# Optimization experiments

Measured on AMD Instinct MI355X. Metric: run time of the kernel, lower is better.

The kernel has to match this reference:

```python
import jax, jax.numpy as jnp
import numpy as np

B, N, IN_DIM, HID = 8, 4096, 256, 256


def setup_inputs() -> dict:
    key = jax.random.key(0)
    ks = jax.random.split(key, 7)
    s_in = 1.0 / np.sqrt(IN_DIM)
    return {
        "x": jax.random.normal(ks[0], (B, N, IN_DIM), dtype=jnp.float32),
        "Wq": jax.random.uniform(ks[1], (IN_DIM, HID), jnp.float32, -s_in, s_in),
        "bq": jax.random.uniform(ks[2], (HID,), jnp.float32, -s_in, s_in),
        "Wk": jax.random.uniform(ks[3], (IN_DIM, HID), jnp.float32, -s_in, s_in),
        "bk": jax.random.uniform(ks[4], (HID,), jnp.float32, -s_in, s_in),
        "Wv": jax.random.uniform(ks[5], (IN_DIM, HID), jnp.float32, -s_in, s_in),
        "bv": jax.random.uniform(ks[6], (HID,), jnp.float32, -s_in, s_in),
    }


def reference(x, Wq, bq, Wk, bk, Wv, bv):
    # x: [B, N, in_dim]
    Q = jnp.einsum("bnd,dh->bnh", x, Wq) + bq  # [B, N, H]
    K = jnp.einsum("bnd,dh->bnh", x, Wk) + bk
    V = jnp.einsum("bnd,dh->bnh", x, Wv) + bv
    scale = 1.0 / jnp.sqrt(jnp.asarray(K.shape[-1], dtype=x.dtype))
    scores = jnp.einsum("bqh,bkh->bqk", Q, K) * scale  # [B, N, N]
    attn = jax.nn.softmax(scores, axis=-1)
    out = jnp.einsum("bqk,bkh->bqh", attn, V)  # [B, N, H]
    return out.mean(axis=1)  # [B, H]
```

## Files before the change

kernel.cpp:

```cpp
#include <hip/hip_runtime.h>
#include <hip/hip_bf16.h>


#define NTOK 4096
#define HDIM 256
#define NBATCH 8
#define SCALE 0.0625f

typedef __attribute__((ext_vector_type(8))) short short8_t;
typedef __attribute__((ext_vector_type(16))) float f32x16;

__device__ __forceinline__ unsigned short f2bf(float f) {
    unsigned u = __float_as_uint(f);
    u += 0x7fff + ((u >> 16) & 1);
    return (unsigned short)(u >> 16);
}

#define MFMA(a, b, c) __builtin_amdgcn_mfma_f32_32x32x16_bf16(a, b, c, 0, 0, 0)

__device__ __forceinline__ void async_cp16(const void* g, void* l) {
    __builtin_amdgcn_global_load_lds((const __attribute__((address_space(1))) void*)g,
                                     (__attribute__((address_space(3))) void*)l, 16, 0, 0);
}

__device__ __forceinline__ void stage_swz(unsigned short* lds, const unsigned short* src,
                                          int row0, int dbase, int w, int l) {
#pragma unroll
    for (int i = 0; i < 4; ++i) {
        int rloc = w * 32 + i * 8 + (l >> 3);
        int u = (l & 7) ^ (l >> 3);
        const unsigned short* g = src + (size_t)(row0 + rloc) * HDIM + dbase + u * 8;
        unsigned short* d = lds + (w * 32 + i * 8) * 64;
        async_cp16(g, d);
    }
}

__device__ __forceinline__ short8_t frd(const unsigned short* lds, int rb, int lo, int u) {
    return *(const short8_t*)(lds + ((rb * 32 + lo) * 8 + (u ^ (lo & 7))) * 8);
}

__global__ void zero_kernel(float* __restrict__ w, float* __restrict__ l, float* __restrict__ out) {
    int i = blockIdx.x * 256 + threadIdx.x;
    w[i] = 0.f;
    l[i] = 0.f;
    if (i < NBATCH * HDIM) out[i] = 0.f;
}

__global__ void convert_wt(const float* __restrict__ Wq, const float* __restrict__ Wk,
                           const float* __restrict__ Wv, unsigned short* __restrict__ Wt) {
    int z = blockIdx.y;
    const float* W = (z == 0) ? Wq : (z == 1) ? Wk : Wv;
    unsigned short* o = Wt + z * 65536;
    int n = threadIdx.x;
    for (int kk = 0; kk < 32; ++kk) {
        int k = blockIdx.x * 32 + kk;
        o[n * 256 + k] = f2bf(W[k * 256 + n]);
    }
}

__device__ __forceinline__ void stage_tile(unsigned short* __restrict__ dst,
                                           const unsigned short* __restrict__ src,
                                           int row0, int dbase, int t) {
#pragma unroll
    for (int i = 0; i < 4; ++i) {
        int f = t + i * 256;
        int r = f >> 3;
        int c8 = (f & 7) * 8;
        *(uint4*)(dst + r * 72 + c8) = *(const uint4*)(src + (size_t)(row0 + r) * HDIM + dbase + c8);
    }
}

__global__ __launch_bounds__(256) void qkv_mfma(const float* __restrict__ x,
                                                const unsigned short* __restrict__ Wt,
                                                const float* __restrict__ bq, const float* __restrict__ bk,
                                                const float* __restrict__ bv,
                                                unsigned short* __restrict__ Qbf,
                                                unsigned short* __restrict__ Kbf,
                                                float* __restrict__ Vf) {
    const int z = blockIdx.z;
    const unsigned short* Wz = Wt + z * 65536;
    const float* bias = (z == 0) ? bq : (z == 1) ? bk : bv;
    const int m0 = blockIdx.x * 128, n0 = blockIdx.y * 128;
    const int t = threadIdx.x, wv_ = t >> 6, l = t & 63, lo = l & 31, hi = l >> 5;
    const int wq = (wv_ & 1) * 64, wk = (wv_ >> 1) * 64;

    __shared__ __align__(16) char smem[36864];
    unsigned short* Xs = (unsigned short*)smem;
    unsigned short* Ws = Xs + 128 * 72;

    f32x16 acc[2][2];
#pragma unroll
    for (int a = 0; a < 2; ++a)
#pragma unroll
        for (int b = 0; b < 2; ++b)
#pragma unroll
            for (int r = 0; r < 16; ++r) acc[a][b][r] = 0.f;

    for (int dc = 0; dc < 4; ++dc) {
        __syncthreads();
#pragma unroll
        for (int i = 0; i < 4; ++i) {
            int f = t + i * 256;
            int r = f >> 3;
            int c8 = (f & 7) * 8;
            const float* s = x + (size_t)(m0 + r) * HDIM + dc * 64 + c8;
            float4 v0 = *(const float4*)s;
            float4 v1 = *(const float4*)(s + 4);
            short8_t o;
            o[0] = (short)f2bf(v0.x); o[1] = (short)f2bf(v0.y);
            o[2] = (short)f2bf(v0.z); o[3] = (short)f2bf(v0.w);
            o[4] = (short)f2bf(v1.x); o[5] = (short)f2bf(v1.y);
            o[6] = (short)f2bf(v1.z); o[7] = (short)f2bf(v1.w);
            *(short8_t*)(Xs + r * 72 + c8) = o;
        }
        stage_tile(Ws, Wz, n0, dc * 64, t);
        __syncthreads();
#pragma unroll
        for (int ks = 0; ks < 4; ++ks) {
            int kidx = ks * 16 + hi * 8;
            short8_t a0 = *(const short8_t*)(Xs + (wq + lo) * 72 + kidx);
            short8_t a1 = *(const short8_t*)(Xs + (wq + 32 + lo) * 72 + kidx);
            short8_t b0 = *(const short8_t*)(Ws + (wk + lo) * 72 + kidx);
            short8_t b1 = *(const short8_t*)(Ws + (wk + 32 + lo) * 72 + kidx);
            acc[0][0] = MFMA(a0, b0, acc[0][0]);
            acc[0][1] = MFMA(a0, b1, acc[0][1]);
            acc[1][0] = MFMA(a1, b0, acc[1][0]);
            acc[1][1] = MFMA(a1, b1, acc[1][1]);
        }
    }
    float bc0 = bias[n0 + wk + lo];
    float bc1 = bias[n0 + wk + 32 + lo];
#pragma unroll
    for (int mb = 0; mb < 2; ++mb)
#pragma unroll
        for (int r = 0; r < 16; ++r) {
            int row = m0 + wq + mb * 32 + (r & 3) + 8 * (r >> 2) + 4 * hi;
            int c0 = n0 + wk + lo, c1 = n0 + wk + 32 + lo;
            float v0 = acc[mb][0][r] + bc0;
            float v1 = acc[mb][1][r] + bc1;
            if (z == 2) {
                Vf[(size_t)row * HDIM + c0] = v0;
                Vf[(size_t)row * HDIM + c1] = v1;
            } else {
                unsigned short* o = (z == 0) ? Qbf : Kbf;
                o[(size_t)row * HDIM + c0] = f2bf(v0);
                o[(size_t)row * HDIM + c1] = f2bf(v1);
            }
        }
}

__global__ __launch_bounds__(256) void score_pass1(const unsigned short* __restrict__ Qbf,
                                                   const unsigned short* __restrict__ Kbf,
                                                   float* __restrict__ lsum) {
    const int b = blockIdx.z;
    const int q0 = blockIdx.x * 128;
    const int kslice = blockIdx.y;
    const int t = threadIdx.x, w = t >> 6, l = t & 63, lo = l & 31, hi = l >> 5;
    const int rq = (w & 1) * 2, rk = (w >> 1) * 2;
    const unsigned short* Qb = Qbf + (size_t)b * NTOK * HDIM;
    const unsigned short* Kb = Kbf + (size_t)b * NTOK * HDIM;

    __shared__ __align__(16) char smem[33792];
    unsigned short* Qs = (unsigned short*)smem;
    unsigned short* Ks = Qs + 8192;
    float* red = (float*)smem;

    float rs[2][16];
#pragma unroll
    for (int mb = 0; mb < 2; ++mb)
#pragma unroll
        for (int r = 0; r < 16; ++r) rs[mb][r] = 0.f;

    for (int kt = 0; kt < 4; ++kt) {
        const int k0 = kslice * 512 + kt * 128;
        f32x16 acc[2][2];
#pragma unroll
        for (int a = 0; a < 2; ++a)
#pragma unroll
            for (int c = 0; c < 2; ++c)
#pragma unroll
                for (int r = 0; r < 16; ++r) acc[a][c][r] = 0.f;

        for (int dc = 0; dc < 4; ++dc) {
            __syncthreads();
            stage_swz(Qs, Qb, q0, dc * 64, w, l);
            stage_swz(Ks, Kb, k0, dc * 64, w, l);
            __syncthreads();
#pragma unroll
            for (int ks = 0; ks < 4; ++ks) {
                int u = ks * 2 + hi;
                short8_t a0 = frd(Qs, rq + 0, lo, u);
                short8_t a1 = frd(Qs, rq + 1, lo, u);
                short8_t b0 = frd(Ks, rk + 0, lo, u);
                short8_t b1 = frd(Ks, rk + 1, lo, u);
                acc[0][0] = MFMA(a0, b0, acc[0][0]);
                acc[0][1] = MFMA(a0, b1, acc[0][1]);
                acc[1][0] = MFMA(a1, b0, acc[1][0]);
                acc[1][1] = MFMA(a1, b1, acc[1][1]);
            }
        }
#pragma unroll
        for (int mb = 0; mb < 2; ++mb)
#pragma unroll
            for (int r = 0; r < 16; ++r)
                rs[mb][r] += __expf(acc[mb][0][r] * SCALE) + __expf(acc[mb][1][r] * SCALE);
    }
    __syncthreads();
#pragma unroll
    for (int mb = 0; mb < 2; ++mb)
#pragma unroll
        for (int r = 0; r < 16; ++r) {
            int row = (w & 1) * 64 + mb * 32 + (r & 3) + 8 * (r >> 2) + 4 * hi;
            red[row * 66 + (w >> 1) * 32 + lo] = rs[mb][r];
        }
    __syncthreads();
    if (t < 128) {
        float s = 0.f;
#pragma unroll 8
        for (int j = 0; j < 64; ++j) s += red[t * 66 + j];
        atomicAdd(&lsum[b * NTOK + q0 + t], s);
    }
}

__global__ __launch_bounds__(256) void score_pass2(const unsigned short* __restrict__ Qbf,
                                                   const unsigned short* __restrict__ Kbf,
                                                   const float* __restrict__ lsum,
                                                   float* __restrict__ wsum) {
    const int b = blockIdx.z;
    const int k0 = blockIdx.x * 128;
    const int qslice = blockIdx.y;
    const int t = threadIdx.x, w = t >> 6, l = t & 63, lo = l & 31, hi = l >> 5;
    const int rq = (w & 1) * 2, rk = (w >> 1) * 2;
    const unsigned short* Qb = Qbf + (size_t)b * NTOK * HDIM;
    const unsigned short* Kb = Kbf + (size_t)b * NTOK * HDIM;

    __shared__ __align__(16) char smem[33792];
    __shared__ float linv_s[128];
    unsigned short* Qs = (unsigned short*)smem;
    unsigned short* Ks = Qs + 8192;
    float* red2 = (float*)smem;

    float cs0 = 0.f, cs1 = 0.f;

    for (int qt = 0; qt < 4; ++qt) {
        const int q0 = qslice * 512 + qt * 128;
        f32x16 acc[2][2];
#pragma unroll
        for (int a = 0; a < 2; ++a)
#pragma unroll
            for (int c = 0; c < 2; ++c)
#pragma unroll
                for (int r = 0; r < 16; ++r) acc[a][c][r] = 0.f;

        for (int dc = 0; dc < 4; ++dc) {
            __syncthreads();
            stage_swz(Qs, Qb, q0, dc * 64, w, l);
            stage_swz(Ks, Kb, k0, dc * 64, w, l);
            if (dc == 0 && t < 128) linv_s[t] = 1.0f / lsum[b * NTOK + q0 + t];
            __syncthreads();
#pragma unroll
            for (int ks = 0; ks < 4; ++ks) {
                int u = ks * 2 + hi;
                short8_t a0 = frd(Qs, rq + 0, lo, u);
                short8_t a1 = frd(Qs, rq + 1, lo, u);
                short8_t b0 = frd(Ks, rk + 0, lo, u);
                short8_t b1 = frd(Ks, rk + 1, lo, u);
                acc[0][0] = MFMA(a0, b0, acc[0][0]);
                acc[0][1] = MFMA(a0, b1, acc[0][1]);
                acc[1][0] = MFMA(a1, b0, acc[1][0]);
                acc[1][1] = MFMA(a1, b1, acc[1][1]);
            }
        }
#pragma unroll
        for (int mb = 0; mb < 2; ++mb)
#pragma unroll
            for (int r = 0; r < 16; ++r) {
                float li = linv_s[(w & 1) * 64 + mb * 32 + (r & 3) + 8 * (r >> 2) + 4 * hi];
                cs0 += __expf(acc[mb][0][r] * SCALE) * li;
                cs1 += __expf(acc[mb][1][r] * SCALE) * li;
            }
    }
    __syncthreads();
    red2[((w >> 1) * 64 + lo) * 5 + (w & 1) * 2 + hi] = cs0;
    red2[((w >> 1) * 64 + 32 + lo) * 5 + (w & 1) * 2 + hi] = cs1;
    __syncthreads();
    if (t < 128) {
        float s = red2[t * 5 + 0] + red2[t * 5 + 1] + red2[t * 5 + 2] + red2[t * 5 + 3];
        atomicAdd(&wsum[b * NTOK + k0 + t], s);
    }
}

__global__ __launch_bounds__(256) void finalize_kernel(const float* __restrict__ V,
                                                       const float* __restrict__ w,
                                                       float* __restrict__ out) {
    const int b = blockIdx.y;
    const int k0 = blockIdx.x * 256;
    const int h = threadIdx.x;
    __shared__ float wsh[256];
    wsh[h] = w[b * NTOK + k0 + h];
    __syncthreads();
    const float* Vb = V + ((size_t)b * NTOK + k0) * HDIM;
    float acc = 0.f;
#pragma unroll 4
    for (int kk = 0; kk < 256; ++kk) acc = fmaf(wsh[kk], Vb[(size_t)kk * HDIM + h], acc);
    atomicAdd(&out[b * HDIM + h], acc * (1.0f / (float)NTOK));
}

extern "C" void kernel_launch(void* const* d_in, const int* in_sizes, int n_in,
                              void* d_out, int out_size, void* d_ws, size_t ws_size,
                              hipStream_t stream) {
    const float* x  = (const float*)d_in[0];
    const float* Wq = (const float*)d_in[1];
    const float* bq = (const float*)d_in[2];
    const float* Wk = (const float*)d_in[3];
    const float* bk = (const float*)d_in[4];
    const float* Wv = (const float*)d_in[5];
    const float* bv = (const float*)d_in[6];
    float* out = (float*)d_out;

    const size_t BNH = (size_t)NBATCH * NTOK * HDIM;
    unsigned short* Wt  = (unsigned short*)d_ws;
    unsigned short* Qbf = Wt + 3 * 65536;
    unsigned short* Kbf = Qbf + BNH;
    float* Vf   = (float*)(Kbf + BNH);
    float* lsum = Vf + BNH;
    float* wsum = lsum + (size_t)NBATCH * NTOK;

    zero_kernel<<<dim3(128), dim3(256), 0, stream>>>(wsum, lsum, out);
    convert_wt<<<dim3(8, 3), dim3(256), 0, stream>>>(Wq, Wk, Wv, Wt);
    qkv_mfma<<<dim3(256, 2, 3), dim3(256), 0, stream>>>(x, Wt, bq, bk, bv, Qbf, Kbf, Vf);
    score_pass1<<<dim3(32, 8, 8), dim3(256), 0, stream>>>(Qbf, Kbf, lsum);
    score_pass2<<<dim3(32, 8, 8), dim3(256), 0, stream>>>(Qbf, Kbf, lsum, wsum);
    finalize_kernel<<<dim3(16, 8), dim3(256), 0, stream>>>(Vf, wsum, out);
}
```

Measured before the change: 310.6 us.

## Double-buffer Q/K LDS tiles in both score passes to overlap loads with MFMA

Both score kernels now keep two LDS buffers for the Q and K tiles. Each iteration issues the async global-to-LDS copy for the next 64-wide d-chunk before running the MFMAs on the current one, so each step needs one barrier instead of two. The inverse row-sum buffer in pass 2 is double-buffered the same way. In exchange, LDS per block doubles to 64KB, which can reduce how many blocks fit on a CU.

```diff
diff --git a/kernel.cpp b/kernel.cpp
--- a/kernel.cpp
+++ b/kernel.cpp
@@ -154,15 +154,13 @@
                                                    float* __restrict__ lsum) {
     const int b = blockIdx.z;
     const int q0 = blockIdx.x * 128;
-    const int kslice = blockIdx.y;
+    const int kbase = blockIdx.y * 512;
     const int t = threadIdx.x, w = t >> 6, l = t & 63, lo = l & 31, hi = l >> 5;
     const int rq = (w & 1) * 2, rk = (w >> 1) * 2;
     const unsigned short* Qb = Qbf + (size_t)b * NTOK * HDIM;
     const unsigned short* Kb = Kbf + (size_t)b * NTOK * HDIM;
 
-    __shared__ __align__(16) char smem[33792];
-    unsigned short* Qs = (unsigned short*)smem;
-    unsigned short* Ks = Qs + 8192;
+    __shared__ __align__(16) char smem[65536];
     float* red = (float*)smem;
 
     float rs[2][16];
@@ -171,41 +169,51 @@
 #pragma unroll
         for (int r = 0; r < 16; ++r) rs[mb][r] = 0.f;
 
-    for (int kt = 0; kt < 4; ++kt) {
-        const int k0 = kslice * 512 + kt * 128;
-        f32x16 acc[2][2];
-#pragma unroll
-        for (int a = 0; a < 2; ++a)
-#pragma unroll
-            for (int c = 0; c < 2; ++c)
-#pragma unroll
-                for (int r = 0; r < 16; ++r) acc[a][c][r] = 0.f;
-
-        for (int dc = 0; dc < 4; ++dc) {
-            __syncthreads();
-            stage_swz(Qs, Qb, q0, dc * 64, w, l);
-            stage_swz(Ks, Kb, k0, dc * 64, w, l);
-            __syncthreads();
-#pragma unroll
-            for (int ks = 0; ks < 4; ++ks) {
-                int u = ks * 2 + hi;
-                short8_t a0 = frd(Qs, rq + 0, lo, u);
-                short8_t a1 = frd(Qs, rq + 1, lo, u);
-                short8_t b0 = frd(Ks, rk + 0, lo, u);
-                short8_t b1 = frd(Ks, rk + 1, lo, u);
-                acc[0][0] = MFMA(a0, b0, acc[0][0]);
-                acc[0][1] = MFMA(a0, b1, acc[0][1]);
-                acc[1][0] = MFMA(a1, b0, acc[1][0]);
-                acc[1][1] = MFMA(a1, b1, acc[1][1]);
-            }
-        }
-#pragma unroll
-        for (int mb = 0; mb < 2; ++mb)
-#pragma unroll
-            for (int r = 0; r < 16; ++r)
-                rs[mb][r] += __expf(acc[mb][0][r] * SCALE) + __expf(acc[mb][1][r] * SCALE);
-    }
-    __syncthreads();
+    f32x16 acc[2][2];
+
+    stage_swz((unsigned short*)smem, Qb, q0, 0, w, l);
+    stage_swz((unsigned short*)(smem + 32768), Kb, kbase, 0, w, l);
+    __syncthreads();
+
+    for (int s = 0; s < 16; ++s) {
+        const int dc = s & 3;
+        if (dc == 0) {
+#pragma unroll
+            for (int a = 0; a < 2; ++a)
+#pragma unroll
+                for (int c = 0; c < 2; ++c)
+#pragma unroll
+                    for (int r = 0; r < 16; ++r) acc[a][c][r] = 0.f;
+        }
+        if (s + 1 < 16) {
+            const int s1 = s + 1, kt1 = s1 >> 2, dc1 = s1 & 3;
+            stage_swz((unsigned short*)(smem + (s1 & 1) * 16384), Qb, q0, dc1 * 64, w, l);
+            stage_swz((unsigned short*)(smem + 32768 + (s1 & 1) * 16384), Kb,
+                      kbase + kt1 * 128, dc1 * 64, w, l);
+        }
+        const unsigned short* Qs = (const unsigned short*)(smem + (s & 1) * 16384);
+        const unsigned short* Ks = (const unsigned short*)(smem + 32768 + (s & 1) * 16384);
+#pragma unroll
+        for (int ks = 0; ks < 4; ++ks) {
+            int u = ks * 2 + hi;
+            short8_t a0 = frd(Qs, rq + 0, lo, u);
+            short8_t a1 = frd(Qs, rq + 1, lo, u);
+            short8_t b0 = frd(Ks, rk + 0, lo, u);
+            short8_t b1 = frd(Ks, rk + 1, lo, u);
+            acc[0][0] = MFMA(a0, b0, acc[0][0]);
+            acc[0][1] = MFMA(a0, b1, acc[0][1]);
+            acc[1][0] = MFMA(a1, b0, acc[1][0]);
+            acc[1][1] = MFMA(a1, b1, acc[1][1]);
+        }
+        if (dc == 3) {
+#pragma unroll
+            for (int mb = 0; mb < 2; ++mb)
+#pragma unroll
+                for (int r = 0; r < 16; ++r)
+                    rs[mb][r] += __expf(acc[mb][0][r] * SCALE) + __expf(acc[mb][1][r] * SCALE);
+        }
+        __syncthreads();
+    }
 #pragma unroll
     for (int mb = 0; mb < 2; ++mb)
 #pragma unroll
@@ -228,59 +236,69 @@
                                                    float* __restrict__ wsum) {
     const int b = blockIdx.z;
     const int k0 = blockIdx.x * 128;
-    const int qslice = blockIdx.y;
+    const int qbase = blockIdx.y * 512;
     const int t = threadIdx.x, w = t >> 6, l = t & 63, lo = l & 31, hi = l >> 5;
     const int rq = (w & 1) * 2, rk = (w >> 1) * 2;
     const unsigned short* Qb = Qbf + (size_t)b * NTOK * HDIM;
     const unsigned short* Kb = Kbf + (size_t)b * NTOK * HDIM;
 
-    __shared__ __align__(16) char smem[33792];
-    __shared__ float linv_s[128];
-    unsigned short* Qs = (unsigned short*)smem;
-    unsigned short* Ks = Qs + 8192;
+    __shared__ __align__(16) char smem[65536];
+    __shared__ float linv_s[2][128];
     float* red2 = (float*)smem;
 
     float cs0 = 0.f, cs1 = 0.f;
-
-    for (int qt = 0; qt < 4; ++qt) {
-        const int q0 = qslice * 512 + qt * 128;
-        f32x16 acc[2][2];
-#pragma unroll
-        for (int a = 0; a < 2; ++a)
-#pragma unroll
-            for (int c = 0; c < 2; ++c)
-#pragma unroll
-                for (int r = 0; r < 16; ++r) acc[a][c][r] = 0.f;
-
-        for (int dc = 0; dc < 4; ++dc) {
-            __syncthreads();
-            stage_swz(Qs, Qb, q0, dc * 64, w, l);
-            stage_swz(Ks, Kb, k0, dc * 64, w, l);
-            if (dc == 0 && t < 128) linv_s[t] = 1.0f / lsum[b * NTOK + q0 + t];
-            __syncthreads();
-#pragma unroll
-            for (int ks = 0; ks < 4; ++ks) {
-                int u = ks * 2 + hi;
-                short8_t a0 = frd(Qs, rq + 0, lo, u);
-                short8_t a1 = frd(Qs, rq + 1, lo, u);
-                short8_t b0 = frd(Ks, rk + 0, lo, u);
-                short8_t b1 = frd(Ks, rk + 1, lo, u);
-                acc[0][0] = MFMA(a0, b0, acc[0][0]);
-                acc[0][1] = MFMA(a0, b1, acc[0][1]);
-                acc[1][0] = MFMA(a1, b0, acc[1][0]);
-                acc[1][1] = MFMA(a1, b1, acc[1][1]);
-            }
-        }
-#pragma unroll
-        for (int mb = 0; mb < 2; ++mb)
-#pragma unroll
-            for (int r = 0; r < 16; ++r) {
-                float li = linv_s[(w & 1) * 64 + mb * 32 + (r & 3) + 8 * (r >> 2) + 4 * hi];
-                cs0 += __expf(acc[mb][0][r] * SCALE) * li;
-                cs1 += __expf(acc[mb][1][r] * SCALE) * li;
-            }
-    }
-    __syncthreads();
+    f32x16 acc[2][2];
+
+    stage_swz((unsigned short*)smem, Qb, qbase, 0, w, l);
+    stage_swz((unsigned short*)(smem + 32768), Kb, k0, 0, w, l);
+    if (t < 128) linv_s[0][t] = 1.0f / lsum[b * NTOK + qbase + t];
+    __syncthreads();
+
+    for (int s = 0; s < 16; ++s) {
+        const int kt = s >> 2, dc = s & 3;
+        if (dc == 0) {
+#pragma unroll
+            for (int a = 0; a < 2; ++a)
+#pragma unroll
+                for (int c = 0; c < 2; ++c)
+#pragma unroll
+                    for (int r = 0; r < 16; ++r) acc[a][c][r] = 0.f;
+        }
+        if (s + 1 < 16) {
+            const int s1 = s + 1, kt1 = s1 >> 2, dc1 = s1 & 3;
+            stage_swz((unsigned short*)(smem + (s1 & 1) * 16384), Qb,
+                      qbase + kt1 * 128, dc1 * 64, w, l);
+            stage_swz((unsigned short*)(smem + 32768 + (s1 & 1) * 16384), Kb,
+                      k0, dc1 * 64, w, l);
+            if (dc1 == 0 && t < 128)
+                linv_s[kt1 & 1][t] = 1.0f / lsum[b * NTOK + qbase + kt1 * 128 + t];
+        }
+        const unsigned short* Qs = (const unsigned short*)(smem + (s & 1) * 16384);
+        const unsigned short* Ks = (const unsigned short*)(smem + 32768 + (s & 1) * 16384);
+#pragma unroll
+        for (int ks = 0; ks < 4; ++ks) {
+            int u = ks * 2 + hi;
+            short8_t a0 = frd(Qs, rq + 0, lo, u);
+            short8_t a1 = frd(Qs, rq + 1, lo, u);
+            short8_t b0 = frd(Ks, rk + 0, lo, u);
+            short8_t b1 = frd(Ks, rk + 1, lo, u);
+            acc[0][0] = MFMA(a0, b0, acc[0][0]);
+            acc[0][1] = MFMA(a0, b1, acc[0][1]);
+            acc[1][0] = MFMA(a1, b0, acc[1][0]);
+            acc[1][1] = MFMA(a1, b1, acc[1][1]);
+        }
+        if (dc == 3) {
+#pragma unroll
+            for (int mb = 0; mb < 2; ++mb)
+#pragma unroll
+                for (int r = 0; r < 16; ++r) {
+                    float li = linv_s[kt & 1][(w & 1) * 64 + mb * 32 + (r & 3) + 8 * (r >> 2) + 4 * hi];
+                    cs0 += __expf(acc[mb][0][r] * SCALE) * li;
+                    cs1 += __expf(acc[mb][1][r] * SCALE) * li;
+                }
+        }
+        __syncthreads();
+    }
     red2[((w >> 1) * 64 + lo) * 5 + (w & 1) * 2 + hi] = cs0;
     red2[((w >> 1) * 64 + 32 + lo) * 5 + (w & 1) * 2 + hi] = cs1;
     __syncthreads();
```

Result: slower. 361.0 us (+16.2%).

## Preconvert x to bf16 and stage QKV tiles via async swizzled LDS loads

Applied to the files above, without the earlier changes.

Adds a separate kernel that converts x to bf16 once, so the QKV GEMM no longer reads fp32 x and converts it six times (once per block in y and z). The GEMM now stages both the X and W tiles with global_load_lds async copies into an XOR-swizzled LDS layout, replacing padded register-staged copies. This halves the bytes of x read per GEMM block, at the cost of an extra pass that writes and then rereads a 16 MB bf16 buffer, plus more workspace.

```diff
diff --git a/kernel.cpp b/kernel.cpp
--- a/kernel.cpp
+++ b/kernel.cpp
@@ -44,6 +44,14 @@
     w[i] = 0.f;
     l[i] = 0.f;
     if (i < NBATCH * HDIM) out[i] = 0.f;
+}
+
+__global__ void convert_x(const float* __restrict__ x, unsigned short* __restrict__ xbf) {
+    int i = (blockIdx.x * 256 + threadIdx.x) * 4;
+    float4 v = *(const float4*)(x + i);
+    ushort4 o;
+    o.x = f2bf(v.x); o.y = f2bf(v.y); o.z = f2bf(v.z); o.w = f2bf(v.w);
+    *(ushort4*)(xbf + i) = o;
 }
 
 __global__ void convert_wt(const float* __restrict__ Wq, const float* __restrict__ Wk,
@@ -58,19 +66,7 @@
     }
 }
 
-__device__ __forceinline__ void stage_tile(unsigned short* __restrict__ dst,
-                                           const unsigned short* __restrict__ src,
-                                           int row0, int dbase, int t) {
-#pragma unroll
-    for (int i = 0; i < 4; ++i) {
-        int f = t + i * 256;
-        int r = f >> 3;
-        int c8 = (f & 7) * 8;
-        *(uint4*)(dst + r * 72 + c8) = *(const uint4*)(src + (size_t)(row0 + r) * HDIM + dbase + c8);
-    }
-}
-
-__global__ __launch_bounds__(256) void qkv_mfma(const float* __restrict__ x,
+__global__ __launch_bounds__(256) void qkv_mfma(const unsigned short* __restrict__ xbf,
                                                 const unsigned short* __restrict__ Wt,
                                                 const float* __restrict__ bq, const float* __restrict__ bk,
                                                 const float* __restrict__ bv,
@@ -81,61 +77,47 @@
     const unsigned short* Wz = Wt + z * 65536;
     const float* bias = (z == 0) ? bq : (z == 1) ? bk : bv;
     const int m0 = blockIdx.x * 128, n0 = blockIdx.y * 128;
-    const int t = threadIdx.x, wv_ = t >> 6, l = t & 63, lo = l & 31, hi = l >> 5;
-    const int wq = (wv_ & 1) * 64, wk = (wv_ >> 1) * 64;
-
-    __shared__ __align__(16) char smem[36864];
-    unsigned short* Xs = (unsigned short*)smem;
-    unsigned short* Ws = Xs + 128 * 72;
+    const int t = threadIdx.x, w = t >> 6, l = t & 63, lo = l & 31, hi = l >> 5;
+    const int rm = (w & 1) * 2, rn = (w >> 1) * 2;
+
+    __shared__ __align__(16) char smem[32768];
+    unsigned short* Xb = (unsigned short*)smem;
+    unsigned short* Wb = (unsigned short*)(smem + 16384);
 
     f32x16 acc[2][2];
 #pragma unroll
     for (int a = 0; a < 2; ++a)
 #pragma unroll
-        for (int b = 0; b < 2; ++b)
-#pragma unroll
-            for (int r = 0; r < 16; ++r) acc[a][b][r] = 0.f;
+        for (int c = 0; c < 2; ++c)
+#pragma unroll
+            for (int r = 0; r < 16; ++r) acc[a][c][r] = 0.f;
 
     for (int dc = 0; dc < 4; ++dc) {
         __syncthreads();
-#pragma unroll
-        for (int i = 0; i < 4; ++i) {
-            int f = t + i * 256;
-            int r = f >> 3;
-            int c8 = (f & 7) * 8;
-            const float* s = x + (size_t)(m0 + r) * HDIM + dc * 64 + c8;
-            float4 v0 = *(const float4*)s;
-            float4 v1 = *(const float4*)(s + 4);
-            short8_t o;
-            o[0] = (short)f2bf(v0.x); o[1] = (short)f2bf(v0.y);
-            o[2] = (short)f2bf(v0.z); o[3] = (short)f2bf(v0.w);
-            o[4] = (short)f2bf(v1.x); o[5] = (short)f2bf(v1.y);
-            o[6] = (short)f2bf(v1.z); o[7] = (short)f2bf(v1.w);
-            *(short8_t*)(Xs + r * 72 + c8) = o;
-        }
-        stage_tile(Ws, Wz, n0, dc * 64, t);
+        stage_swz(Xb, xbf, m0, dc * 64, w, l);
+        stage_swz(Wb, Wz, n0, dc * 64, w, l);
         __syncthreads();
 #pragma unroll
         for (int ks = 0; ks < 4; ++ks) {
-            int kidx = ks * 16 + hi * 8;
-            short8_t a0 = *(const short8_t*)(Xs + (wq + lo) * 72 + kidx);
-            short8_t a1 = *(const short8_t*)(Xs + (wq + 32 + lo) * 72 + kidx);
-            short8_t b0 = *(const short8_t*)(Ws + (wk + lo) * 72 + kidx);
-            short8_t b1 = *(const short8_t*)(Ws + (wk + 32 + lo) * 72 + kidx);
+            int u = ks * 2 + hi;
+            short8_t a0 = frd(Xb, rm + 0, lo, u);
+            short8_t a1 = frd(Xb, rm + 1, lo, u);
+            short8_t b0 = frd(Wb, rn + 0, lo, u);
+            short8_t b1 = frd(Wb, rn + 1, lo, u);
             acc[0][0] = MFMA(a0, b0, acc[0][0]);
             acc[0][1] = MFMA(a0, b1, acc[0][1]);
             acc[1][0] = MFMA(a1, b0, acc[1][0]);
             acc[1][1] = MFMA(a1, b1, acc[1][1]);
         }
     }
-    float bc0 = bias[n0 + wk + lo];
-    float bc1 = bias[n0 + wk + 32 + lo];
+    float bc0 = bias[n0 + (w >> 1) * 64 + lo];
+    float bc1 = bias[n0 + (w >> 1) * 64 + 32 + lo];
 #pragma unroll
     for (int mb = 0; mb < 2; ++mb)
 #pragma unroll
         for (int r = 0; r < 16; ++r) {
-            int row = m0 + wq + mb * 32 + (r & 3) + 8 * (r >> 2) + 4 * hi;
-            int c0 = n0 + wk + lo, c1 = n0 + wk + 32 + lo;
+            int row = m0 + (w & 1) * 64 + mb * 32 + (r & 3) + 8 * (r >> 2) + 4 * hi;
+            int c0 = n0 + (w >> 1) * 64 + lo, c1 = c0 + 32;
             float v0 = acc[mb][0][r] + bc0;
             float v1 = acc[mb][1][r] + bc1;
             if (z == 2) {
@@ -320,15 +302,17 @@
 
     const size_t BNH = (size_t)NBATCH * NTOK * HDIM;
     unsigned short* Wt  = (unsigned short*)d_ws;
-    unsigned short* Qbf = Wt + 3 * 65536;
+    unsigned short* xbf = Wt + 3 * 65536;
+    unsigned short* Qbf = xbf + BNH;
     unsigned short* Kbf = Qbf + BNH;
     float* Vf   = (float*)(Kbf + BNH);
     float* lsum = Vf + BNH;
     float* wsum = lsum + (size_t)NBATCH * NTOK;
 
     zero_kernel<<<dim3(128), dim3(256), 0, stream>>>(wsum, lsum, out);
+    convert_x<<<dim3(8192), dim3(256), 0, stream>>>(x, xbf);
     convert_wt<<<dim3(8, 3), dim3(256), 0, stream>>>(Wq, Wk, Wv, Wt);
-    qkv_mfma<<<dim3(256, 2, 3), dim3(256), 0, stream>>>(x, Wt, bq, bk, bv, Qbf, Kbf, Vf);
+    qkv_mfma<<<dim3(256, 2, 3), dim3(256), 0, stream>>>(xbf, Wt, bq, bk, bv, Qbf, Kbf, Vf);
     score_pass1<<<dim3(32, 8, 8), dim3(256), 0, stream>>>(Qbf, Kbf, lsum);
     score_pass2<<<dim3(32, 8, 8), dim3(256), 0, stream>>>(Qbf, Kbf, lsum, wsum);
     finalize_kernel<<<dim3(16, 8), dim3(256), 0, stream>>>(Vf, wsum, out);
```

Result: faster. 294.6 us (-5.2%).
